# Optimization experiments

Hardware: AMD Instinct MI355X
Metric: run time of the kernel (lower is better)

Reference implementation:

```python
import jax, jax.numpy as jnp
import numpy as np

NU = 200000   # num user nodes
NI = 200000   # num item nodes
E = 500000    # edges per relation
D = 128       # in_feats
H = 128       # h_feats
NEG_SLOPE = 0.01  # F.leaky_relu default


def _sage(x_src, x_dst, src, dst, n_dst, W_self, W_neigh, b):
    # DGL SAGEConv('mean'): fc_self(x_dst) + fc_neigh(mean of in-neighbors) + bias
    msg = x_src[src]                                   # [E, d] gather
    agg = jax.ops.segment_sum(msg, dst, num_segments=n_dst)   # [n_dst, d]
    deg = jax.ops.segment_sum(jnp.ones((src.shape[0],), x_src.dtype), dst,
                              num_segments=n_dst)      # [n_dst]
    mean = agg / jnp.maximum(deg, 1.0)[:, None]        # zero in-degree -> 0
    return x_dst @ W_self + mean @ W_neigh + b


def setup_inputs() -> dict:
    key = jax.random.key(0)
    ks = jax.random.split(key, 20)
    s = 1.0 / np.sqrt(D)
    inp = {
        'x_user': jax.random.normal(ks[0], (NU, D), jnp.float32),
        'x_item': jax.random.normal(ks[1], (NI, D), jnp.float32),
        'w1_self_uc': jax.random.normal(ks[2], (D, H), jnp.float32) * s,
        'w1_neigh_uc': jax.random.normal(ks[3], (D, H), jnp.float32) * s,
        'b1_uc': jnp.zeros((H,), jnp.float32),
        'w1_self_iu': jax.random.normal(ks[4], (D, H), jnp.float32) * s,
        'w1_neigh_iu': jax.random.normal(ks[5], (D, H), jnp.float32) * s,
        'b1_iu': jnp.zeros((H,), jnp.float32),
        'w2_self_uc': jax.random.normal(ks[6], (H, H), jnp.float32) * s,
        'w2_neigh_uc': jax.random.normal(ks[7], (H, H), jnp.float32) * s,
        'b2_uc': jnp.zeros((H,), jnp.float32),
        'w2_self_iu': jax.random.normal(ks[8], (H, H), jnp.float32) * s,
        'w2_neigh_iu': jax.random.normal(ks[9], (H, H), jnp.float32) * s,
        'b2_iu': jnp.zeros((H,), jnp.float32),
        'src_uc': jax.random.randint(ks[10], (E,), 0, NU, jnp.int32),
        'dst_uc': jax.random.randint(ks[11], (E,), 0, NI, jnp.int32),
        'src_iu': jax.random.randint(ks[12], (E,), 0, NI, jnp.int32),
        'dst_iu': jax.random.randint(ks[13], (E,), 0, NU, jnp.int32),
    }
    return inp


def reference(x_user, x_item,
              w1_self_uc, w1_neigh_uc, b1_uc, w1_self_iu, w1_neigh_iu, b1_iu,
              w2_self_uc, w2_neigh_uc, b2_uc, w2_self_iu, w2_neigh_iu, b2_iu,
              src_uc, dst_uc, src_iu, dst_iu):
    # layer 1: relation 'clicks' user->item, relation 'clicked_by' item->user
    h1_item = _sage(x_user, x_item, src_uc, dst_uc, NI, w1_self_uc, w1_neigh_uc, b1_uc)
    h1_user = _sage(x_item, x_user, src_iu, dst_iu, NU, w1_self_iu, w1_neigh_iu, b1_iu)
    h1_item = jax.nn.leaky_relu(h1_item, NEG_SLOPE)
    h1_user = jax.nn.leaky_relu(h1_user, NEG_SLOPE)
    # layer 2
    h2_item = _sage(h1_user, h1_item, src_uc, dst_uc, NI, w2_self_uc, w2_neigh_uc, b2_uc)
    h2_user = _sage(h1_item, h1_user, src_iu, dst_iu, NU, w2_self_iu, w2_neigh_iu, b2_iu)
    # stack [user, item] (same shape) for a single output tensor
    return jnp.stack([h2_user, h2_item], axis=0)  # [2, 200000, 128]
```

## Files before the change

kernel.cpp:

```cpp
#include <hip/hip_runtime.h>
#include <hip/hip_bf16.h>

#define D_ 128

typedef __attribute__((ext_vector_type(8))) short s8b;
typedef __attribute__((ext_vector_type(4))) float f4;

union U4 { uint u[4]; s8b v; uint4 q; };

__device__ __forceinline__ void gl16(const void* g, void* lds) {
    __builtin_amdgcn_global_load_lds(
        (const __attribute__((address_space(1))) void*)g,
        (__attribute__((address_space(3))) void*)lds, 16, 0, 0);
}

__device__ __forceinline__ void split2(float f0, float f1, uint& hp, uint& lp) {
    uint u0 = __float_as_uint(f0), u1 = __float_as_uint(f1);
    hp = (u0 >> 16) | (u1 & 0xffff0000u);
    float r0 = f0 - __uint_as_float(u0 & 0xffff0000u);
    float r1 = f1 - __uint_as_float(u1 & 0xffff0000u);
    uint v0 = __float_as_uint(r0), v1 = __float_as_uint(r1);
    uint l0 = (v0 + 0x7fffu + ((v0 >> 16) & 1u)) >> 16;
    uint l1 = (v1 + 0x7fffu + ((v1 >> 16) & 1u)) >> 16;
    lp = l0 | (l1 << 16);
}

__global__ void deg2_kernel(const int* __restrict__ dstA, const int* __restrict__ dstB,
                            int* __restrict__ degA, int* __restrict__ degB, int E) {
    int e = blockIdx.x * blockDim.x + threadIdx.x;
    const int* dst = blockIdx.y ? dstB : dstA;
    int* deg = blockIdx.y ? degB : degA;
    if (e < E) atomicAdd(&deg[dst[e]], 1);
}

__global__ __launch_bounds__(256)
void scan1m(const int* __restrict__ degA, const int* __restrict__ degB,
            int* __restrict__ rpA, int* __restrict__ rpB,
            int* __restrict__ partA, int* __restrict__ partB, int N) {
    const int* deg = blockIdx.y ? degB : degA;
    int* rp = blockIdx.y ? rpB : rpA;
    int* partials = blockIdx.y ? partB : partA;
    int tid = threadIdx.x;
    int i = blockIdx.x * 256 + tid;
    int v = (i < N) ? deg[i] : 0;
    int lane = tid & 63, wid = tid >> 6;
    int x = v;
#pragma unroll
    for (int off = 1; off < 64; off <<= 1) {
        int y = __shfl_up(x, off, 64);
        if (lane >= off) x += y;
    }
    __shared__ int wsum[5];
    if (lane == 63) wsum[wid] = x;
    __syncthreads();
    if (tid == 0) {
        int a = wsum[0], b = wsum[1], c = wsum[2], d = wsum[3];
        wsum[0] = 0; wsum[1] = a; wsum[2] = a + b; wsum[3] = a + b + c;
        wsum[4] = a + b + c + d;
    }
    __syncthreads();
    if (i < N) rp[i] = wsum[wid] + x - v;
    if (tid == 0) partials[blockIdx.x] = wsum[4];
}

__global__ __launch_bounds__(1024)
void scan2m(int* __restrict__ partA, int* __restrict__ partB, int B) {
    int* partials = blockIdx.x ? partB : partA;
    __shared__ int buf[1024];
    int t = threadIdx.x;
    int v = (t < B) ? partials[t] : 0;
    buf[t] = v;
    __syncthreads();
    for (int off = 1; off < 1024; off <<= 1) {
        int add = (t >= off) ? buf[t - off] : 0;
        __syncthreads();
        buf[t] += add;
        __syncthreads();
    }
    if (t < B) partials[t] = buf[t] - v;
}

__global__ __launch_bounds__(256)
void scan3m(int* __restrict__ rpA, int* __restrict__ rpB,
            const int* __restrict__ partA, const int* __restrict__ partB, int N, int E) {
    int* rp = blockIdx.y ? rpB : rpA;
    const int* partials = blockIdx.y ? partB : partA;
    int i = blockIdx.x * 256 + threadIdx.x;
    if (i < N) rp[i] += partials[blockIdx.x];
    if (i == 0) rp[N] = E;
}

__global__ void fill2_csr(const int* __restrict__ srcA, const int* __restrict__ dstA,
                          const int* __restrict__ rpA, int* __restrict__ curA,
                          int* __restrict__ colA, int* __restrict__ colpA,
                          const int* __restrict__ srcB, const int* __restrict__ dstB,
                          const int* __restrict__ rpB, int* __restrict__ curB,
                          int* __restrict__ colB, int* __restrict__ colpB, int E) {
    int e = blockIdx.x * blockDim.x + threadIdx.x;
    if (e >= E) return;
    const int* src = blockIdx.y ? srcB : srcA;
    const int* dst = blockIdx.y ? dstB : dstA;
    const int* rp  = blockIdx.y ? rpB : rpA;
    int* cursor = blockIdx.y ? curB : curA;
    int* col    = blockIdx.y ? colB : colA;
    int* colp   = blockIdx.y ? colpB : colpA;
    int d = dst[e];
    int s = src[e];
    int idx = atomicAdd(&cursor[d], 1);
    col[rp[d] + idx] = s;
    if (idx < 4) colp[d * 4 + idx] = s;
}

__device__ __forceinline__ void acc8hl(float* a, uint4 h4, uint4 l4, float wgt) {
    const ushort* hu = (const ushort*)&h4;
    const ushort* lu = (const ushort*)&l4;
#pragma unroll
    for (int j = 0; j < 8; ++j) {
        float v = __uint_as_float((uint)hu[j] << 16) + __uint_as_float((uint)lu[j] << 16);
        a[j] = fmaf(v, wgt, a[j]);
    }
}
__device__ __forceinline__ void acc8f(float* a, float4 u0, float4 u1, float wgt) {
    a[0] = fmaf(u0.x, wgt, a[0]); a[1] = fmaf(u0.y, wgt, a[1]);
    a[2] = fmaf(u0.z, wgt, a[2]); a[3] = fmaf(u0.w, wgt, a[3]);
    a[4] = fmaf(u1.x, wgt, a[4]); a[5] = fmaf(u1.y, wgt, a[5]);
    a[6] = fmaf(u1.z, wgt, a[6]); a[7] = fmaf(u1.w, wgt, a[7]);
}

template<int INHL>
__device__ __forceinline__ void gather_node(const char* x, const int* rp,
        const int* col, const int* colp, ushort* out, int node, int li) {
    int beg = rp[node], end = rp[node + 1];
    int dg = end - beg;
    int4 c4 = *(const int4*)(colp + (size_t)node * 4);
    int s0 = dg > 0 ? c4.x : 0;
    int s1 = dg > 1 ? c4.y : 0;
    int s2 = dg > 2 ? c4.z : 0;
    int s3 = dg > 3 ? c4.w : 0;
    float w0 = dg > 0 ? 1.f : 0.f;
    float w1 = dg > 1 ? 1.f : 0.f;
    float w2 = dg > 2 ? 1.f : 0.f;
    float w3 = dg > 3 ? 1.f : 0.f;
    float a[8];
#pragma unroll
    for (int j = 0; j < 8; ++j) a[j] = 0.f;

    if (INHL) {
        const char* p0 = x + (size_t)s0 * 512 + li * 16;
        const char* p1 = x + (size_t)s1 * 512 + li * 16;
        const char* p2 = x + (size_t)s2 * 512 + li * 16;
        const char* p3 = x + (size_t)s3 * 512 + li * 16;
        uint4 H0 = *(const uint4*)p0, L0 = *(const uint4*)(p0 + 256);
        uint4 H1 = *(const uint4*)p1, L1 = *(const uint4*)(p1 + 256);
        uint4 H2 = *(const uint4*)p2, L2 = *(const uint4*)(p2 + 256);
        uint4 H3 = *(const uint4*)p3, L3 = *(const uint4*)(p3 + 256);
        acc8hl(a, H0, L0, w0); acc8hl(a, H1, L1, w1);
        acc8hl(a, H2, L2, w2); acc8hl(a, H3, L3, w3);
    } else {
        const char* p0 = x + (size_t)s0 * 512 + li * 32;
        const char* p1 = x + (size_t)s1 * 512 + li * 32;
        const char* p2 = x + (size_t)s2 * 512 + li * 32;
        const char* p3 = x + (size_t)s3 * 512 + li * 32;
        float4 A0 = *(const float4*)p0, B0 = *(const float4*)(p0 + 16);
        float4 A1 = *(const float4*)p1, B1 = *(const float4*)(p1 + 16);
        float4 A2 = *(const float4*)p2, B2 = *(const float4*)(p2 + 16);
        float4 A3 = *(const float4*)p3, B3 = *(const float4*)(p3 + 16);
        acc8f(a, A0, B0, w0); acc8f(a, A1, B1, w1);
        acc8f(a, A2, B2, w2); acc8f(a, A3, B3, w3);
    }
    for (int e = beg + 4; e < end; ++e) {
        int s = col[e];
        if (INHL) {
            const char* p = x + (size_t)s * 512 + li * 16;
            acc8hl(a, *(const uint4*)p, *(const uint4*)(p + 256), 1.f);
        } else {
            const char* p = x + (size_t)s * 512 + li * 32;
            acc8f(a, *(const float4*)p, *(const float4*)(p + 16), 1.f);
        }
    }
    float inv = 1.f / (float)(dg > 0 ? dg : 1);
    uint h0, h1, h2, h3, l0, l1, l2, l3;
    split2(a[0] * inv, a[1] * inv, h0, l0);
    split2(a[2] * inv, a[3] * inv, h1, l1);
    split2(a[4] * inv, a[5] * inv, h2, l2);
    split2(a[6] * inv, a[7] * inv, h3, l3);
    char* ob = (char*)out + (size_t)node * 512;
    *(uint4*)(ob + li * 16) = make_uint4(h0, h1, h2, h3);
    *(uint4*)(ob + 256 + li * 16) = make_uint4(l0, l1, l2, l3);
}

template<int INHL>
__global__ __launch_bounds__(256)
void gather2k(const void* xA, const int* rpA, const int* colA, const int* colpA,
              ushort* outA, int NA,
              const void* xB, const int* rpB, const int* colB, const int* colpB,
              ushort* outB, int NB, int blocksA) {
    bool isA = (int)blockIdx.x < blocksA;
    int bid = isA ? blockIdx.x : blockIdx.x - blocksA;
    long long gid = (long long)bid * 256 + threadIdx.x;
    int node = (int)(gid >> 4);
    int li = (int)(gid & 15);
    if (isA) { if (node < NA) gather_node<INHL>((const char*)xA, rpA, colA, colpA, outA, node, li); }
    else     { if (node < NB) gather_node<INHL>((const char*)xB, rpB, colB, colpB, outB, node, li); }
}

__global__ __launch_bounds__(256)
void prep_weights(const float* __restrict__ s0, const float* __restrict__ n0,
                  const float* __restrict__ s1, const float* __restrict__ n1,
                  const float* __restrict__ s2, const float* __restrict__ n2,
                  const float* __restrict__ s3, const float* __restrict__ n3,
                  ushort* __restrict__ WTH, ushort* __restrict__ WTL) {
    int g = blockIdx.y;
    int t = blockIdx.x * 256 + threadIdx.x;
    int c = t & 127;
    int oct = t >> 7;
    const float* self  = g == 0 ? s0 : g == 1 ? s1 : g == 2 ? s2 : s3;
    const float* neigh = g == 0 ? n0 : g == 1 ? n1 : g == 2 ? n2 : n3;
    uint hd[4], ld_[4];
#pragma unroll
    for (int p = 0; p < 4; ++p) {
        uint hpair = 0, lpair = 0;
#pragma unroll
        for (int q = 0; q < 2; ++q) {
            int kv = oct * 8 + p * 2 + q;
            const float* Wsrc = kv < 128 ? self : neigh;
            float f = Wsrc[(size_t)(kv & 127) * 128 + c];
            uint u = __float_as_uint(f);
            uint h = u >> 16;
            float r = f - __uint_as_float(u & 0xffff0000u);
            uint v = __float_as_uint(r);
            uint l = (v + 0x7fffu + ((v >> 16) & 1u)) >> 16;
            hpair |= h << (16 * q);
            lpair |= l << (16 * q);
        }
        hd[p] = hpair; ld_[p] = lpair;
    }
    size_t base = ((size_t)g * 128 + c) * 256 + oct * 8;
    *(uint4*)(WTH + base) = make_uint4(hd[0], hd[1], hd[2], hd[3]);
    *(uint4*)(WTL + base) = make_uint4(ld_[0], ld_[1], ld_[2], ld_[3]);
}

template<int A1FP32, int SPLIT, int LRELU>
__device__ __forceinline__ void gemm_body(const void* A1, const void* A2,
        const ushort* WTh, const ushort* WTl, const float* bias, void* outp,
        int N, int bid, char* smem) {
    const int t = threadIdx.x;
    const int w = t >> 6, lane = t & 63;
    const int fr = lane & 15, hi = lane >> 4;
    const int mrow0 = (w & 1) * 32, ncol0 = (w >> 1) * 64;
    const int row0 = bid * 64;

    f4 acc[2][4];
    {
        float bv[4];
#pragma unroll
        for (int n = 0; n < 4; ++n) bv[n] = bias[ncol0 + n * 16 + fr];
#pragma unroll
        for (int m = 0; m < 2; ++m)
#pragma unroll
            for (int n = 0; n < 4; ++n) acc[m][n] = (f4){bv[n], bv[n], bv[n], bv[n]};
    }

    for (int ks = 0; ks < 8; ++ks) {
        if (A1FP32 && ks < 4) {
            const char* src = (const char*)A1;
#pragma unroll
            for (int it = 0; it < 2; ++it) {
                int j = it * 256 + t;
                int row = j >> 3, cs = j & 7;
                int gr = row0 + row; gr = gr < N ? gr : N - 1;
                gl16(src + (size_t)gr * 512 + ks * 128 + ((cs ^ (row & 7)) * 16),
                     smem + j * 16);
            }
        } else {
            const char* src = (ks < 4) ? (const char*)A1 : (const char*)A2;
            const int kk = ks & 3;
            {
                int j = t;
                int row = j >> 2, cs = j & 3;
                int gr = row0 + row; gr = gr < N ? gr : N - 1;
                size_t so = (size_t)gr * 512 + kk * 64 + ((cs ^ ((row >> 1) & 3)) * 16);
                gl16(src + so, smem + j * 16);
                gl16(src + so + 256, smem + 4096 + j * 16);
            }
        }
        {
#pragma unroll
            for (int it = 0; it < 2; ++it) {
                int j = it * 256 + t;
                int col = j >> 2, cs = j & 3;
                size_t so = (size_t)col * 512 + ks * 64 + ((cs ^ ((col >> 1) & 3)) * 16);
                gl16((const char*)WTh + so, smem + 8192 + j * 16);
                gl16((const char*)WTl + so, smem + 16384 + j * 16);
            }
        }
        __syncthreads();

        s8b ah[2], al[2], wh[4], wl[4];
        if (A1FP32 && ks < 4) {
#pragma unroll
            for (int m = 0; m < 2; ++m) {
                int r = mrow0 + m * 16 + fr;
                f4 x0 = *(const f4*)(smem + r * 128 + (((hi * 2) ^ (r & 7)) * 16));
                f4 x1 = *(const f4*)(smem + r * 128 + (((hi * 2 + 1) ^ (r & 7)) * 16));
                U4 H, L;
                split2(x0[0], x0[1], H.u[0], L.u[0]);
                split2(x0[2], x0[3], H.u[1], L.u[1]);
                split2(x1[0], x1[1], H.u[2], L.u[2]);
                split2(x1[2], x1[3], H.u[3], L.u[3]);
                ah[m] = H.v; al[m] = L.v;
            }
        } else {
#pragma unroll
            for (int m = 0; m < 2; ++m) {
                int r = mrow0 + m * 16 + fr;
                int off = r * 64 + ((hi ^ ((r >> 1) & 3)) * 16);
                ah[m] = *(const s8b*)(smem + off);
                al[m] = *(const s8b*)(smem + 4096 + off);
            }
        }
#pragma unroll
        for (int n = 0; n < 4; ++n) {
            int c = ncol0 + n * 16 + fr;
            int off = c * 64 + ((hi ^ ((c >> 1) & 3)) * 16);
            wh[n] = *(const s8b*)(smem + 8192 + off);
            wl[n] = *(const s8b*)(smem + 16384 + off);
        }
#pragma unroll
        for (int n = 0; n < 4; ++n)
#pragma unroll
            for (int m = 0; m < 2; ++m) {
                acc[m][n] = __builtin_amdgcn_mfma_f32_16x16x32_bf16(ah[m], wh[n], acc[m][n], 0, 0, 0);
                acc[m][n] = __builtin_amdgcn_mfma_f32_16x16x32_bf16(al[m], wh[n], acc[m][n], 0, 0, 0);
                acc[m][n] = __builtin_amdgcn_mfma_f32_16x16x32_bf16(ah[m], wl[n], acc[m][n], 0, 0, 0);
            }
        __syncthreads();
    }

    float* T = (float*)smem;
#pragma unroll
    for (int m = 0; m < 2; ++m)
#pragma unroll
        for (int n = 0; n < 4; ++n)
#pragma unroll
            for (int r = 0; r < 4; ++r)
                T[(mrow0 + m * 16 + hi * 4 + r) * 132 + ncol0 + n * 16 + fr] = acc[m][n][r];
    __syncthreads();
    {
        int row = t >> 2, q = t & 3;
        int gr = row0 + row;
        if (gr < N) {
            if (SPLIT) {
                char* ob = (char*)outp + (size_t)gr * 512;
#pragma unroll
                for (int i = 0; i < 4; ++i) {
                    const float* p = T + row * 132 + i * 32 + q * 8;
                    f4 x0 = *(const f4*)p;
                    f4 x1 = *(const f4*)(p + 4);
                    float e[8] = {x0[0], x0[1], x0[2], x0[3], x1[0], x1[1], x1[2], x1[3]};
                    if (LRELU) {
#pragma unroll
                        for (int j = 0; j < 8; ++j) e[j] = e[j] > 0.f ? e[j] : 0.01f * e[j];
                    }
                    uint h[4], l[4];
#pragma unroll
                    for (int j = 0; j < 4; ++j) split2(e[2 * j], e[2 * j + 1], h[j], l[j]);
                    *(uint4*)(ob + i * 64 + q * 16) = make_uint4(h[0], h[1], h[2], h[3]);
                    *(uint4*)(ob + 256 + i * 64 + q * 16) = make_uint4(l[0], l[1], l[2], l[3]);
                }
            } else {
                float* ob = (float*)outp + (size_t)gr * 128;
#pragma unroll
                for (int i = 0; i < 8; ++i) {
                    f4 x = *(const f4*)(T + row * 132 + i * 16 + q * 4);
                    float e0 = x[0], e1 = x[1], e2 = x[2], e3 = x[3];
                    if (LRELU) {
                        e0 = e0 > 0.f ? e0 : 0.01f * e0;
                        e1 = e1 > 0.f ? e1 : 0.01f * e1;
                        e2 = e2 > 0.f ? e2 : 0.01f * e2;
                        e3 = e3 > 0.f ? e3 : 0.01f * e3;
                    }
                    *(float4*)(ob + i * 16 + q * 4) = make_float4(e0, e1, e2, e3);
                }
            }
        }
    }
}

template<int A1FP32, int SPLIT, int LRELU>
__global__ __launch_bounds__(256, 4)
void gemm2k(const void* A1a, const void* A2a, const ushort* WTha, const ushort* WTla,
            const float* ba, void* outa, int Na,
            const void* A1b, const void* A2b, const ushort* WThb, const ushort* WTlb,
            const float* bb, void* outb, int Nb, int blocksA) {
    __shared__ __align__(16) char smem[33792];
    bool isA = (int)blockIdx.x < blocksA;
    int bid = isA ? blockIdx.x : blockIdx.x - blocksA;
    if (isA) gemm_body<A1FP32, SPLIT, LRELU>(A1a, A2a, WTha, WTla, ba, outa, Na, bid, smem);
    else     gemm_body<A1FP32, SPLIT, LRELU>(A1b, A2b, WThb, WTlb, bb, outb, Nb, bid, smem);
}

extern "C" void kernel_launch(void* const* d_in, const int* in_sizes, int n_in,
                              void* d_out, int out_size, void* d_ws, size_t ws_size,
                              hipStream_t stream) {
    const float* x_user     = (const float*)d_in[0];
    const float* x_item     = (const float*)d_in[1];
    const float* w1_self_uc = (const float*)d_in[2];
    const float* w1_neigh_uc= (const float*)d_in[3];
    const float* b1_uc      = (const float*)d_in[4];
    const float* w1_self_iu = (const float*)d_in[5];
    const float* w1_neigh_iu= (const float*)d_in[6];
    const float* b1_iu      = (const float*)d_in[7];
    const float* w2_self_uc = (const float*)d_in[8];
    const float* w2_neigh_uc= (const float*)d_in[9];
    const float* b2_uc      = (const float*)d_in[10];
    const float* w2_self_iu = (const float*)d_in[11];
    const float* w2_neigh_iu= (const float*)d_in[12];
    const float* b2_iu      = (const float*)d_in[13];
    const int* src_uc = (const int*)d_in[14];
    const int* dst_uc = (const int*)d_in[15];
    const int* src_iu = (const int*)d_in[16];
    const int* dst_iu = (const int*)d_in[17];

    const int NU = in_sizes[0] / D_;
    const int NI = in_sizes[1] / D_;
    const int E  = in_sizes[14];

    char* hl_user = (char*)d_out;
    char* hl_item = (char*)d_out + (size_t)NU * 512;
    float* f_user = (float*)d_out;
    float* f_item = (float*)d_out + (size_t)NU * 128;

    char* ws = (char*)d_ws;
    const size_t FEAT_BYTES = (size_t)200000 * 512;
    ushort* agg_i  = (ushort*)ws; ws += FEAT_BYTES;
    ushort* agg_u  = (ushort*)ws; ws += FEAT_BYTES;
    ushort* WTH    = (ushort*)ws; ws += (size_t)4 * 128 * 256 * sizeof(ushort);
    ushort* WTL    = (ushort*)ws; ws += (size_t)4 * 128 * 256 * sizeof(ushort);
    int* colp_uc   = (int*)ws;    ws += (size_t)200000 * 4 * sizeof(int);
    int* colp_iu   = (int*)ws;    ws += (size_t)200000 * 4 * sizeof(int);
    int* rp_uc     = (int*)ws;    ws += (size_t)(NI + 1) * sizeof(int);
    int* rp_iu     = (int*)ws;    ws += (size_t)(NU + 1) * sizeof(int);
    int* col_uc    = (int*)ws;    ws += (size_t)E * sizeof(int);
    int* col_iu    = (int*)ws;    ws += (size_t)E * sizeof(int);
    int* deg_uc    = (int*)ws;    ws += (size_t)200000 * sizeof(int);
    int* deg_iu    = (int*)ws;    ws += (size_t)200000 * sizeof(int);
    int* cur_uc    = (int*)ws;    ws += (size_t)200000 * sizeof(int);
    int* cur_iu    = (int*)ws;    ws += (size_t)200000 * sizeof(int);
    int* partA     = (int*)ws;    ws += (size_t)1024 * sizeof(int);
    int* partB     = (int*)ws;    ws += (size_t)1024 * sizeof(int);

    const int TPB = 256;
    const int eBlocks  = (E + TPB - 1) / TPB;
    const int sBlocks  = (200000 + 255) / 256;
    const int gBlocksI = (int)(((long long)NI * 16 + TPB - 1) / TPB);
    const int gBlocksU = (int)(((long long)NU * 16 + TPB - 1) / TPB);
    const int mBlocksI = (NI + 63) / 64;
    const int mBlocksU = (NU + 63) / 64;
    const size_t WSTRIDE = (size_t)128 * 256;

    hipMemsetAsync(deg_uc, 0, (size_t)4 * 200000 * sizeof(int), stream);

    prep_weights<<<dim3(16, 4), 256, 0, stream>>>(
        w1_self_uc, w1_neigh_uc, w1_self_iu, w1_neigh_iu,
        w2_self_uc, w2_neigh_uc, w2_self_iu, w2_neigh_iu, WTH, WTL);

    deg2_kernel<<<dim3(eBlocks, 2), TPB, 0, stream>>>(dst_uc, dst_iu, deg_uc, deg_iu, E);
    scan1m<<<dim3(sBlocks, 2), 256, 0, stream>>>(deg_uc, deg_iu, rp_uc, rp_iu, partA, partB, 200000);
    scan2m<<<2, 1024, 0, stream>>>(partA, partB, sBlocks);
    scan3m<<<dim3(sBlocks, 2), 256, 0, stream>>>(rp_uc, rp_iu, partA, partB, 200000, E);
    fill2_csr<<<dim3(eBlocks, 2), TPB, 0, stream>>>(src_uc, dst_uc, rp_uc, cur_uc, col_uc, colp_uc,
                                                    src_iu, dst_iu, rp_iu, cur_iu, col_iu, colp_iu, E);

    gather2k<0><<<gBlocksI + gBlocksU, TPB, 0, stream>>>(
        x_user, rp_uc, col_uc, colp_uc, agg_i, NI,
        x_item, rp_iu, col_iu, colp_iu, agg_u, NU, gBlocksI);
    gemm2k<1, 1, 1><<<mBlocksI + mBlocksU, TPB, 0, stream>>>(
        x_item, agg_i, WTH + 0 * WSTRIDE, WTL + 0 * WSTRIDE, b1_uc, hl_item, NI,
        x_user, agg_u, WTH + 1 * WSTRIDE, WTL + 1 * WSTRIDE, b1_iu, hl_user, NU,
        mBlocksI);

    gather2k<1><<<gBlocksI + gBlocksU, TPB, 0, stream>>>(
        hl_user, rp_uc, col_uc, colp_uc, agg_i, NI,
        hl_item, rp_iu, col_iu, colp_iu, agg_u, NU, gBlocksI);
    gemm2k<0, 0, 0><<<mBlocksI + mBlocksU, TPB, 0, stream>>>(
        hl_item, agg_i, WTH + 2 * WSTRIDE, WTL + 2 * WSTRIDE, b2_uc, f_item, NI,
        hl_user, agg_u, WTH + 3 * WSTRIDE, WTL + 3 * WSTRIDE, b2_iu, f_user, NU,
        mBlocksI);
}
```

Baseline: 617.5 us.

## Fuse neighbor mean-gather into SAGE GEMM kernel via LDS staging

Replaces the separate gather and GEMM kernels with one fused kernel per layer. Each 512-thread block gathers the mean neighbor features for its 64 rows, splits them into hi/lo bf16, and writes them to a swizzled LDS buffer, which the MFMA GEMM then reads directly. This removes the global write and re-read of the aggregated feature buffers and two launches. In exchange, LDS use per block grows, 8 waves each hold smaller tiles, and the gather latency sits on the GEMM's critical path instead of running as its own fully occupied kernel. Layer-1 outputs now go to workspace rather than to the output buffer, and the N bounds checks were removed, which is safe only because N is a multiple of 64.

```diff
diff --git a/kernel.cpp b/kernel.cpp
--- a/kernel.cpp
+++ b/kernel.cpp
@@ -111,99 +111,6 @@
     if (idx < 4) colp[d * 4 + idx] = s;
 }
 
-__device__ __forceinline__ void acc8hl(float* a, uint4 h4, uint4 l4, float wgt) {
-    const ushort* hu = (const ushort*)&h4;
-    const ushort* lu = (const ushort*)&l4;
-#pragma unroll
-    for (int j = 0; j < 8; ++j) {
-        float v = __uint_as_float((uint)hu[j] << 16) + __uint_as_float((uint)lu[j] << 16);
-        a[j] = fmaf(v, wgt, a[j]);
-    }
-}
-__device__ __forceinline__ void acc8f(float* a, float4 u0, float4 u1, float wgt) {
-    a[0] = fmaf(u0.x, wgt, a[0]); a[1] = fmaf(u0.y, wgt, a[1]);
-    a[2] = fmaf(u0.z, wgt, a[2]); a[3] = fmaf(u0.w, wgt, a[3]);
-    a[4] = fmaf(u1.x, wgt, a[4]); a[5] = fmaf(u1.y, wgt, a[5]);
-    a[6] = fmaf(u1.z, wgt, a[6]); a[7] = fmaf(u1.w, wgt, a[7]);
-}
-
-template<int INHL>
-__device__ __forceinline__ void gather_node(const char* x, const int* rp,
-        const int* col, const int* colp, ushort* out, int node, int li) {
-    int beg = rp[node], end = rp[node + 1];
-    int dg = end - beg;
-    int4 c4 = *(const int4*)(colp + (size_t)node * 4);
-    int s0 = dg > 0 ? c4.x : 0;
-    int s1 = dg > 1 ? c4.y : 0;
-    int s2 = dg > 2 ? c4.z : 0;
-    int s3 = dg > 3 ? c4.w : 0;
-    float w0 = dg > 0 ? 1.f : 0.f;
-    float w1 = dg > 1 ? 1.f : 0.f;
-    float w2 = dg > 2 ? 1.f : 0.f;
-    float w3 = dg > 3 ? 1.f : 0.f;
-    float a[8];
-#pragma unroll
-    for (int j = 0; j < 8; ++j) a[j] = 0.f;
-
-    if (INHL) {
-        const char* p0 = x + (size_t)s0 * 512 + li * 16;
-        const char* p1 = x + (size_t)s1 * 512 + li * 16;
-        const char* p2 = x + (size_t)s2 * 512 + li * 16;
-        const char* p3 = x + (size_t)s3 * 512 + li * 16;
-        uint4 H0 = *(const uint4*)p0, L0 = *(const uint4*)(p0 + 256);
-        uint4 H1 = *(const uint4*)p1, L1 = *(const uint4*)(p1 + 256);
-        uint4 H2 = *(const uint4*)p2, L2 = *(const uint4*)(p2 + 256);
-        uint4 H3 = *(const uint4*)p3, L3 = *(const uint4*)(p3 + 256);
-        acc8hl(a, H0, L0, w0); acc8hl(a, H1, L1, w1);
-        acc8hl(a, H2, L2, w2); acc8hl(a, H3, L3, w3);
-    } else {
-        const char* p0 = x + (size_t)s0 * 512 + li * 32;
-        const char* p1 = x + (size_t)s1 * 512 + li * 32;
-        const char* p2 = x + (size_t)s2 * 512 + li * 32;
-        const char* p3 = x + (size_t)s3 * 512 + li * 32;
-        float4 A0 = *(const float4*)p0, B0 = *(const float4*)(p0 + 16);
-        float4 A1 = *(const float4*)p1, B1 = *(const float4*)(p1 + 16);
-        float4 A2 = *(const float4*)p2, B2 = *(const float4*)(p2 + 16);
-        float4 A3 = *(const float4*)p3, B3 = *(const float4*)(p3 + 16);
-        acc8f(a, A0, B0, w0); acc8f(a, A1, B1, w1);
-        acc8f(a, A2, B2, w2); acc8f(a, A3, B3, w3);
-    }
-    for (int e = beg + 4; e < end; ++e) {
-        int s = col[e];
-        if (INHL) {
-            const char* p = x + (size_t)s * 512 + li * 16;
-            acc8hl(a, *(const uint4*)p, *(const uint4*)(p + 256), 1.f);
-        } else {
-            const char* p = x + (size_t)s * 512 + li * 32;
-            acc8f(a, *(const float4*)p, *(const float4*)(p + 16), 1.f);
-        }
-    }
-    float inv = 1.f / (float)(dg > 0 ? dg : 1);
-    uint h0, h1, h2, h3, l0, l1, l2, l3;
-    split2(a[0] * inv, a[1] * inv, h0, l0);
-    split2(a[2] * inv, a[3] * inv, h1, l1);
-    split2(a[4] * inv, a[5] * inv, h2, l2);
-    split2(a[6] * inv, a[7] * inv, h3, l3);
-    char* ob = (char*)out + (size_t)node * 512;
-    *(uint4*)(ob + li * 16) = make_uint4(h0, h1, h2, h3);
-    *(uint4*)(ob + 256 + li * 16) = make_uint4(l0, l1, l2, l3);
-}
-
-template<int INHL>
-__global__ __launch_bounds__(256)
-void gather2k(const void* xA, const int* rpA, const int* colA, const int* colpA,
-              ushort* outA, int NA,
-              const void* xB, const int* rpB, const int* colB, const int* colpB,
-              ushort* outB, int NB, int blocksA) {
-    bool isA = (int)blockIdx.x < blocksA;
-    int bid = isA ? blockIdx.x : blockIdx.x - blocksA;
-    long long gid = (long long)bid * 256 + threadIdx.x;
-    int node = (int)(gid >> 4);
-    int li = (int)(gid & 15);
-    if (isA) { if (node < NA) gather_node<INHL>((const char*)xA, rpA, colA, colpA, outA, node, li); }
-    else     { if (node < NB) gather_node<INHL>((const char*)xB, rpB, colB, colpB, outB, node, li); }
-}
-
 __global__ __launch_bounds__(256)
 void prep_weights(const float* __restrict__ s0, const float* __restrict__ n0,
                   const float* __restrict__ s1, const float* __restrict__ n1,
@@ -240,94 +147,188 @@
     *(uint4*)(WTL + base) = make_uint4(ld_[0], ld_[1], ld_[2], ld_[3]);
 }
 
-template<int A1FP32, int SPLIT, int LRELU>
-__device__ __forceinline__ void gemm_body(const void* A1, const void* A2,
+#define AGGH 0
+#define AGGL 16384
+#define ASTEP 32768
+#define WHO 40960
+#define WLO 49152
+
+template<int FP32IN, int SPLIT, int LRELU>
+__device__ __forceinline__ void fused_body(const char* A1, const char* XN,
+        const int* rp, const int* col, const int* colp,
         const ushort* WTh, const ushort* WTl, const float* bias, void* outp,
-        int N, int bid, char* smem) {
+        int bid, char* smem) {
     const int t = threadIdx.x;
+    const int row0 = bid * 64;
+
+    {
+        const int li = t & 15;
+#pragma unroll
+        for (int pass = 0; pass < 2; ++pass) {
+            int nl = pass * 32 + (t >> 4);
+            int node = row0 + nl;
+            int beg = rp[node], end = rp[node + 1];
+            int dg = end - beg;
+            int4 c4 = *(const int4*)(colp + (size_t)node * 4);
+            int s0 = dg > 0 ? c4.x : 0;
+            int s1 = dg > 1 ? c4.y : 0;
+            int s2 = dg > 2 ? c4.z : 0;
+            int s3 = dg > 3 ? c4.w : 0;
+            float w0 = dg > 0 ? 1.f : 0.f;
+            float w1 = dg > 1 ? 1.f : 0.f;
+            float w2 = dg > 2 ? 1.f : 0.f;
+            float w3 = dg > 3 ? 1.f : 0.f;
+            float a[8];
+#pragma unroll
+            for (int j = 0; j < 8; ++j) a[j] = 0.f;
+            if (FP32IN) {
+                const char* p0 = XN + (size_t)s0 * 512 + li * 32;
+                const char* p1 = XN + (size_t)s1 * 512 + li * 32;
+                const char* p2 = XN + (size_t)s2 * 512 + li * 32;
+                const char* p3 = XN + (size_t)s3 * 512 + li * 32;
+                float4 A0 = *(const float4*)p0, B0 = *(const float4*)(p0 + 16);
+                float4 A1v = *(const float4*)p1, B1 = *(const float4*)(p1 + 16);
+                float4 A2v = *(const float4*)p2, B2 = *(const float4*)(p2 + 16);
+                float4 A3v = *(const float4*)p3, B3 = *(const float4*)(p3 + 16);
+                float e0[8] = {A0.x, A0.y, A0.z, A0.w, B0.x, B0.y, B0.z, B0.w};
+                float e1[8] = {A1v.x, A1v.y, A1v.z, A1v.w, B1.x, B1.y, B1.z, B1.w};
+                float e2[8] = {A2v.x, A2v.y, A2v.z, A2v.w, B2.x, B2.y, B2.z, B2.w};
+                float e3[8] = {A3v.x, A3v.y, A3v.z, A3v.w, B3.x, B3.y, B3.z, B3.w};
+#pragma unroll
+                for (int j = 0; j < 8; ++j)
+                    a[j] = e0[j] * w0 + e1[j] * w1 + e2[j] * w2 + e3[j] * w3;
+                for (int e = beg + 4; e < end; ++e) {
+                    const char* p = XN + (size_t)col[e] * 512 + li * 32;
+                    float4 X = *(const float4*)p, Y = *(const float4*)(p + 16);
+                    a[0] += X.x; a[1] += X.y; a[2] += X.z; a[3] += X.w;
+                    a[4] += Y.x; a[5] += Y.y; a[6] += Y.z; a[7] += Y.w;
+                }
+            } else {
+                const char* p0 = XN + (size_t)s0 * 512 + li * 16;
+                const char* p1 = XN + (size_t)s1 * 512 + li * 16;
+                const char* p2 = XN + (size_t)s2 * 512 + li * 16;
+                const char* p3 = XN + (size_t)s3 * 512 + li * 16;
+                uint4 H0 = *(const uint4*)p0, L0 = *(const uint4*)(p0 + 256);
+                uint4 H1 = *(const uint4*)p1, L1 = *(const uint4*)(p1 + 256);
+                uint4 H2 = *(const uint4*)p2, L2 = *(const uint4*)(p2 + 256);
+                uint4 H3 = *(const uint4*)p3, L3 = *(const uint4*)(p3 + 256);
+                const ushort* hu; const ushort* lu;
+#pragma unroll
+                for (int q = 0; q < 4; ++q) {
+                    uint4 H = q == 0 ? H0 : q == 1 ? H1 : q == 2 ? H2 : H3;
+                    uint4 L = q == 0 ? L0 : q == 1 ? L1 : q == 2 ? L2 : L3;
+                    float wq = q == 0 ? w0 : q == 1 ? w1 : q == 2 ? w2 : w3;
+                    hu = (const ushort*)&H; lu = (const ushort*)&L;
+#pragma unroll
+                    for (int j = 0; j < 8; ++j) {
+                        float v = __uint_as_float((uint)hu[j] << 16)
+                                + __uint_as_float((uint)lu[j] << 16);
+                        a[j] = fmaf(v, wq, a[j]);
+                    }
+                }
+                for (int e = beg + 4; e < end; ++e) {
+                    const char* p = XN + (size_t)col[e] * 512 + li * 16;
+                    uint4 H = *(const uint4*)p, L = *(const uint4*)(p + 256);
+                    hu = (const ushort*)&H; lu = (const ushort*)&L;
+#pragma unroll
+                    for (int j = 0; j < 8; ++j)
+                        a[j] += __uint_as_float((uint)hu[j] << 16)
+                              + __uint_as_float((uint)lu[j] << 16);
+                }
+            }
+            float inv = 1.f / (float)(dg > 0 ? dg : 1);
+            uint h[4], l[4];
+            split2(a[0] * inv, a[1] * inv, h[0], l[0]);
+            split2(a[2] * inv, a[3] * inv, h[1], l[1]);
+            split2(a[4] * inv, a[5] * inv, h[2], l[2]);
+            split2(a[6] * inv, a[7] * inv, h[3], l[3]);
+            int chunk = li ^ (nl & 3) ^ (((nl >> 2) & 3) << 2);
+            *(uint4*)(smem + AGGH + nl * 256 + chunk * 16) = make_uint4(h[0], h[1], h[2], h[3]);
+            *(uint4*)(smem + AGGL + nl * 256 + chunk * 16) = make_uint4(l[0], l[1], l[2], l[3]);
+        }
+    }
+    __syncthreads();
+
     const int w = t >> 6, lane = t & 63;
     const int fr = lane & 15, hi = lane >> 4;
-    const int mrow0 = (w & 1) * 32, ncol0 = (w >> 1) * 64;
-    const int row0 = bid * 64;
-
-    f4 acc[2][4];
+    const int mrow0 = (w & 1) * 32, ncol0 = (w >> 1) * 32;
+
+    f4 acc[2][2];
     {
-        float bv[4];
-#pragma unroll
-        for (int n = 0; n < 4; ++n) bv[n] = bias[ncol0 + n * 16 + fr];
+        float bv[2];
+#pragma unroll
+        for (int n = 0; n < 2; ++n) bv[n] = bias[ncol0 + n * 16 + fr];
 #pragma unroll
         for (int m = 0; m < 2; ++m)
 #pragma unroll
-            for (int n = 0; n < 4; ++n) acc[m][n] = (f4){bv[n], bv[n], bv[n], bv[n]};
+            for (int n = 0; n < 2; ++n) acc[m][n] = (f4){bv[n], bv[n], bv[n], bv[n]};
     }
 
     for (int ks = 0; ks < 8; ++ks) {
-        if (A1FP32 && ks < 4) {
-            const char* src = (const char*)A1;
-#pragma unroll
-            for (int it = 0; it < 2; ++it) {
-                int j = it * 256 + t;
-                int row = j >> 3, cs = j & 7;
-                int gr = row0 + row; gr = gr < N ? gr : N - 1;
-                gl16(src + (size_t)gr * 512 + ks * 128 + ((cs ^ (row & 7)) * 16),
-                     smem + j * 16);
+        if (ks < 4) {
+            if (FP32IN) {
+                int row = t >> 3, cs = t & 7;
+                gl16(A1 + (size_t)(row0 + row) * 512 + ks * 128 + ((cs ^ (row & 7)) * 16),
+                     smem + ASTEP + t * 16);
+            } else {
+                int j = t & 255, part = t >> 8;
+                int row = j >> 2, cs = j & 3;
+                gl16(A1 + (size_t)(row0 + row) * 512 + part * 256 + ks * 64
+                         + ((cs ^ ((row >> 1) & 3)) * 16),
+                     smem + ASTEP + part * 4096 + j * 16);
+            }
+        }
+        {
+            int col_ = t >> 2, cs = t & 3;
+            size_t so = (size_t)col_ * 512 + ks * 64 + ((cs ^ ((col_ >> 1) & 3)) * 16);
+            gl16((const char*)WTh + so, smem + WHO + t * 16);
+            gl16((const char*)WTl + so, smem + WLO + t * 16);
+        }
+        __syncthreads();
+
+        s8b ah[2], al[2], wh[2], wl[2];
+        if (ks < 4) {
+            if (FP32IN) {
+#pragma unroll
+                for (int m = 0; m < 2; ++m) {
+                    int r = mrow0 + m * 16 + fr;
+                    f4 x0 = *(const f4*)(smem + ASTEP + r * 128 + (((hi * 2) ^ (r & 7)) * 16));
+                    f4 x1 = *(const f4*)(smem + ASTEP + r * 128 + (((hi * 2 + 1) ^ (r & 7)) * 16));
+                    U4 H, L;
+                    split2(x0[0], x0[1], H.u[0], L.u[0]);
+                    split2(x0[2], x0[3], H.u[1], L.u[1]);
+                    split2(x1[0], x1[1], H.u[2], L.u[2]);
+                    split2(x1[2], x1[3], H.u[3], L.u[3]);
+                    ah[m] = H.v; al[m] = L.v;
+                }
+            } else {
+#pragma unroll
+                for (int m = 0; m < 2; ++m) {
+                    int r = mrow0 + m * 16 + fr;
+                    int off = r * 64 + ((hi ^ ((r >> 1) & 3)) * 16);
+                    ah[m] = *(const s8b*)(smem + ASTEP + off);
+                    al[m] = *(const s8b*)(smem + ASTEP + 4096 + off);
+                }
             }
         } else {
-            const char* src = (ks < 4) ? (const char*)A1 : (const char*)A2;
-            const int kk = ks & 3;
-            {
-                int j = t;
-                int row = j >> 2, cs = j & 3;
-                int gr = row0 + row; gr = gr < N ? gr : N - 1;
-                size_t so = (size_t)gr * 512 + kk * 64 + ((cs ^ ((row >> 1) & 3)) * 16);
-                gl16(src + so, smem + j * 16);
-                gl16(src + so + 256, smem + 4096 + j * 16);
-            }
-        }
-        {
-#pragma unroll
-            for (int it = 0; it < 2; ++it) {
-                int j = it * 256 + t;
-                int col = j >> 2, cs = j & 3;
-                size_t so = (size_t)col * 512 + ks * 64 + ((cs ^ ((col >> 1) & 3)) * 16);
-                gl16((const char*)WTh + so, smem + 8192 + j * 16);
-                gl16((const char*)WTl + so, smem + 16384 + j * 16);
-            }
-        }
-        __syncthreads();
-
-        s8b ah[2], al[2], wh[4], wl[4];
-        if (A1FP32 && ks < 4) {
+            int kk = ks - 4;
 #pragma unroll
             for (int m = 0; m < 2; ++m) {
                 int r = mrow0 + m * 16 + fr;
-                f4 x0 = *(const f4*)(smem + r * 128 + (((hi * 2) ^ (r & 7)) * 16));
-                f4 x1 = *(const f4*)(smem + r * 128 + (((hi * 2 + 1) ^ (r & 7)) * 16));
-                U4 H, L;
-                split2(x0[0], x0[1], H.u[0], L.u[0]);
-                split2(x0[2], x0[3], H.u[1], L.u[1]);
-                split2(x1[0], x1[1], H.u[2], L.u[2]);
-                split2(x1[2], x1[3], H.u[3], L.u[3]);
-                ah[m] = H.v; al[m] = L.v;
-            }
-        } else {
-#pragma unroll
-            for (int m = 0; m < 2; ++m) {
-                int r = mrow0 + m * 16 + fr;
-                int off = r * 64 + ((hi ^ ((r >> 1) & 3)) * 16);
-                ah[m] = *(const s8b*)(smem + off);
-                al[m] = *(const s8b*)(smem + 4096 + off);
-            }
-        }
-#pragma unroll
-        for (int n = 0; n < 4; ++n) {
+                int chunk = (kk * 4 + hi) ^ (r & 3) ^ (((r >> 2) & 3) << 2);
+                ah[m] = *(const s8b*)(smem + AGGH + r * 256 + chunk * 16);
+                al[m] = *(const s8b*)(smem + AGGL + r * 256 + chunk * 16);
+            }
+        }
+#pragma unroll
+        for (int n = 0; n < 2; ++n) {
             int c = ncol0 + n * 16 + fr;
             int off = c * 64 + ((hi ^ ((c >> 1) & 3)) * 16);
-            wh[n] = *(const s8b*)(smem + 8192 + off);
-            wl[n] = *(const s8b*)(smem + 16384 + off);
-        }
-#pragma unroll
-        for (int n = 0; n < 4; ++n)
+            wh[n] = *(const s8b*)(smem + WHO + off);
+            wl[n] = *(const s8b*)(smem + WLO + off);
+        }
+#pragma unroll
+        for (int n = 0; n < 2; ++n)
 #pragma unroll
             for (int m = 0; m < 2; ++m) {
                 acc[m][n] = __builtin_amdgcn_mfma_f32_16x16x32_bf16(ah[m], wh[n], acc[m][n], 0, 0, 0);
@@ -341,63 +342,67 @@
 #pragma unroll
     for (int m = 0; m < 2; ++m)
 #pragma unroll
-        for (int n = 0; n < 4; ++n)
+        for (int n = 0; n < 2; ++n)
 #pragma unroll
             for (int r = 0; r < 4; ++r)
                 T[(mrow0 + m * 16 + hi * 4 + r) * 132 + ncol0 + n * 16 + fr] = acc[m][n][r];
     __syncthreads();
     {
-        int row = t >> 2, q = t & 3;
+        int row = t >> 3, q = t & 7;
         int gr = row0 + row;
-        if (gr < N) {
-            if (SPLIT) {
-                char* ob = (char*)outp + (size_t)gr * 512;
-#pragma unroll
-                for (int i = 0; i < 4; ++i) {
-                    const float* p = T + row * 132 + i * 32 + q * 8;
-                    f4 x0 = *(const f4*)p;
-                    f4 x1 = *(const f4*)(p + 4);
-                    float e[8] = {x0[0], x0[1], x0[2], x0[3], x1[0], x1[1], x1[2], x1[3]};
-                    if (LRELU) {
-#pragma unroll
-                        for (int j = 0; j < 8; ++j) e[j] = e[j] > 0.f ? e[j] : 0.01f * e[j];
-                    }
-                    uint h[4], l[4];
-#pragma unroll
-                    for (int j = 0; j < 4; ++j) split2(e[2 * j], e[2 * j + 1], h[j], l[j]);
-                    *(uint4*)(ob + i * 64 + q * 16) = make_uint4(h[0], h[1], h[2], h[3]);
-                    *(uint4*)(ob + 256 + i * 64 + q * 16) = make_uint4(l[0], l[1], l[2], l[3]);
-                }
-            } else {
-                float* ob = (float*)outp + (size_t)gr * 128;
-#pragma unroll
-                for (int i = 0; i < 8; ++i) {
-                    f4 x = *(const f4*)(T + row * 132 + i * 16 + q * 4);
-                    float e0 = x[0], e1 = x[1], e2 = x[2], e3 = x[3];
-                    if (LRELU) {
-                        e0 = e0 > 0.f ? e0 : 0.01f * e0;
-                        e1 = e1 > 0.f ? e1 : 0.01f * e1;
-                        e2 = e2 > 0.f ? e2 : 0.01f * e2;
-                        e3 = e3 > 0.f ? e3 : 0.01f * e3;
-                    }
-                    *(float4*)(ob + i * 16 + q * 4) = make_float4(e0, e1, e2, e3);
-                }
-            }
-        }
-    }
-}
-
-template<int A1FP32, int SPLIT, int LRELU>
-__global__ __launch_bounds__(256, 4)
-void gemm2k(const void* A1a, const void* A2a, const ushort* WTha, const ushort* WTla,
-            const float* ba, void* outa, int Na,
-            const void* A1b, const void* A2b, const ushort* WThb, const ushort* WTlb,
-            const float* bb, void* outb, int Nb, int blocksA) {
-    __shared__ __align__(16) char smem[33792];
+        if (SPLIT) {
+            char* ob = (char*)outp + (size_t)gr * 512;
+#pragma unroll
+            for (int i = 0; i < 2; ++i) {
+                const float* p = T + row * 132 + (q * 2 + i) * 8;
+                f4 x0 = *(const f4*)p;
+                f4 x1 = *(const f4*)(p + 4);
+                float e[8] = {x0[0], x0[1], x0[2], x0[3], x1[0], x1[1], x1[2], x1[3]};
+                if (LRELU) {
+#pragma unroll
+                    for (int j = 0; j < 8; ++j) e[j] = e[j] > 0.f ? e[j] : 0.01f * e[j];
+                }
+                uint h[4], l[4];
+#pragma unroll
+                for (int j = 0; j < 4; ++j) split2(e[2 * j], e[2 * j + 1], h[j], l[j]);
+                *(uint4*)(ob + (q * 2 + i) * 16) = make_uint4(h[0], h[1], h[2], h[3]);
+                *(uint4*)(ob + 256 + (q * 2 + i) * 16) = make_uint4(l[0], l[1], l[2], l[3]);
+            }
+        } else {
+            float* ob = (float*)outp + (size_t)gr * 128;
+#pragma unroll
+            for (int i = 0; i < 4; ++i) {
+                f4 x = *(const f4*)(T + row * 132 + q * 16 + i * 4);
+                float e0 = x[0], e1 = x[1], e2 = x[2], e3 = x[3];
+                if (LRELU) {
+                    e0 = e0 > 0.f ? e0 : 0.01f * e0;
+                    e1 = e1 > 0.f ? e1 : 0.01f * e1;
+                    e2 = e2 > 0.f ? e2 : 0.01f * e2;
+                    e3 = e3 > 0.f ? e3 : 0.01f * e3;
+                }
+                *(float4*)(ob + q * 16 + i * 4) = make_float4(e0, e1, e2, e3);
+            }
+        }
+    }
+}
+
+template<int FP32IN, int SPLIT, int LRELU>
+__global__ __launch_bounds__(512, 2)
+void fused2k(const void* A1a, const void* XNa, const int* rpA, const int* colA,
+             const int* colpA, const ushort* WTha, const ushort* WTla,
+             const float* ba, void* outa,
+             const void* A1b, const void* XNb, const int* rpB, const int* colB,
+             const int* colpB, const ushort* WThb, const ushort* WTlb,
+             const float* bb, void* outb, int blocksA) {
+    __shared__ __align__(16) char smem[57344];
     bool isA = (int)blockIdx.x < blocksA;
     int bid = isA ? blockIdx.x : blockIdx.x - blocksA;
-    if (isA) gemm_body<A1FP32, SPLIT, LRELU>(A1a, A2a, WTha, WTla, ba, outa, Na, bid, smem);
-    else     gemm_body<A1FP32, SPLIT, LRELU>(A1b, A2b, WThb, WTlb, bb, outb, Nb, bid, smem);
+    if (isA)
+        fused_body<FP32IN, SPLIT, LRELU>((const char*)A1a, (const char*)XNa, rpA, colA,
+                                         colpA, WTha, WTla, ba, outa, bid, smem);
+    else
+        fused_body<FP32IN, SPLIT, LRELU>((const char*)A1b, (const char*)XNb, rpB, colB,
+                                         colpB, WThb, WTlb, bb, outb, bid, smem);
 }
 
 extern "C" void kernel_launch(void* const* d_in, const int* in_sizes, int n_in,
@@ -426,15 +431,13 @@
     const int NI = in_sizes[1] / D_;
     const int E  = in_sizes[14];
 
-    char* hl_user = (char*)d_out;
-    char* hl_item = (char*)d_out + (size_t)NU * 512;
     float* f_user = (float*)d_out;
     float* f_item = (float*)d_out + (size_t)NU * 128;
 
     char* ws = (char*)d_ws;
     const size_t FEAT_BYTES = (size_t)200000 * 512;
-    ushort* agg_i  = (ushort*)ws; ws += FEAT_BYTES;
-    ushort* agg_u  = (ushort*)ws; ws += FEAT_BYTES;
+    char* h1_item  = ws;          ws += FEAT_BYTES;
+    char* h1_user  = ws;          ws += FEAT_BYTES;
     ushort* WTH    = (ushort*)ws; ws += (size_t)4 * 128 * 256 * sizeof(ushort);
     ushort* WTL    = (ushort*)ws; ws += (size_t)4 * 128 * 256 * sizeof(ushort);
     int* colp_uc   = (int*)ws;    ws += (size_t)200000 * 4 * sizeof(int);
@@ -453,8 +456,6 @@
     const int TPB = 256;
     const int eBlocks  = (E + TPB - 1) / TPB;
     const int sBlocks  = (200000 + 255) / 256;
-    const int gBlocksI = (int)(((long long)NI * 16 + TPB - 1) / TPB);
-    const int gBlocksU = (int)(((long long)NU * 16 + TPB - 1) / TPB);
     const int mBlocksI = (NI + 63) / 64;
     const int mBlocksU = (NU + 63) / 64;
     const size_t WSTRIDE = (size_t)128 * 256;
@@ -472,19 +473,15 @@
     fill2_csr<<<dim3(eBlocks, 2), TPB, 0, stream>>>(src_uc, dst_uc, rp_uc, cur_uc, col_uc, colp_uc,
                                                     src_iu, dst_iu, rp_iu, cur_iu, col_iu, colp_iu, E);
 
-    gather2k<0><<<gBlocksI + gBlocksU, TPB, 0, stream>>>(
-        x_user, rp_uc, col_uc, colp_uc, agg_i, NI,
-        x_item, rp_iu, col_iu, colp_iu, agg_u, NU, gBlocksI);
-    gemm2k<1, 1, 1><<<mBlocksI + mBlocksU, TPB, 0, stream>>>(
-        x_item, agg_i, WTH + 0 * WSTRIDE, WTL + 0 * WSTRIDE, b1_uc, hl_item, NI,
-        x_user, agg_u, WTH + 1 * WSTRIDE, WTL + 1 * WSTRIDE, b1_iu, hl_user, NU,
-        mBlocksI);
-
-    gather2k<1><<<gBlocksI + gBlocksU, TPB, 0, stream>>>(
-        hl_user, rp_uc, col_uc, colp_uc, agg_i, NI,
-        hl_item, rp_iu, col_iu, colp_iu, agg_u, NU, gBlocksI);
-    gemm2k<0, 0, 0><<<mBlocksI + mBlocksU, TPB, 0, stream>>>(
-        hl_item, agg_i, WTH + 2 * WSTRIDE, WTL + 2 * WSTRIDE, b2_uc, f_item, NI,
-        hl_user, agg_u, WTH + 3 * WSTRIDE, WTL + 3 * WSTRIDE, b2_iu, f_user, NU,
-        mBlocksI);
-}
+    fused2k<1, 1, 1><<<mBlocksI + mBlocksU, 512, 0, stream>>>(
+        x_item, x_user, rp_uc, col_uc, colp_uc, WTH + 0 * WSTRIDE, WTL + 0 * WSTRIDE,
+        b1_uc, h1_item,
+        x_user, x_item, rp_iu, col_iu, colp_iu, WTH + 1 * WSTRIDE, WTL + 1 * WSTRIDE,
+        b1_iu, h1_user, mBlocksI);
+
+    fused2k<0, 0, 0><<<mBlocksI + mBlocksU, 512, 0, stream>>>(
+        h1_item, h1_user, rp_uc, col_uc, colp_uc, WTH + 2 * WSTRIDE, WTL + 2 * WSTRIDE,
+        b2_uc, f_item,
+        h1_user, h1_item, rp_iu, col_iu, colp_iu, WTH + 3 * WSTRIDE, WTL + 3 * WSTRIDE,
+        b2_iu, f_user, mBlocksI);
+}
```

After: 588.4 us. 1.05x faster.
